# Kernel optimization log

Measured on AMD Instinct MI355X. Metric: run time of the kernel, lower is better.

## Reference

```python
import jax, jax.numpy as jnp
import numpy as np

N, E, IN_F, H, F = 4096, 131072, 512, 8, 32  # n_nodes, n_edges, in_features, n_heads, n_hidden
SLOPE = 0.2


def setup_inputs() -> dict:
    key = jax.random.key(0)
    k1, k2, k3, k4 = jax.random.split(key, 4)
    h = jax.random.normal(k1, (N, IN_F), dtype=jnp.float32)
    edge_index = jax.random.randint(k2, (2, E), 0, N)
    train_mask = jnp.ones((E + N,), dtype=jnp.float32)  # mask values written into adj (incl. self-loops appended in forward)
    W_fc = jax.random.normal(k3, (IN_F, H * F), dtype=jnp.float32) * (1.0 / np.sqrt(IN_F))
    W_attn = jax.random.normal(k4, (2 * F,), dtype=jnp.float32) * (1.0 / np.sqrt(2 * F))
    return {"h": h, "edge_index": edge_index, "train_mask": train_mask, "W_fc": W_fc, "W_attn": W_attn}


def reference(h, edge_index, train_mask, W_fc, W_attn):
    n = h.shape[0]
    g = (h @ W_fc).reshape(n, H, F)  # [n, H, F]
    # attn_fc(concat(g_i, g_j)) == g_i @ W_attn[:F] + g_j @ W_attn[F:]  (same math, no NxNx2F tensor)
    el = g @ W_attn[:F]  # [n, H], contribution of source row i
    er = g @ W_attn[F:]  # [n, H], contribution of column j
    e = jax.nn.leaky_relu(el[:, None, :] + er[None, :, :], SLOPE)  # [n, n, H]
    # adjacency: edges (+ self-loops appended in forward) get train_mask values, then diagonal forced to 1
    src = jnp.concatenate([edge_index[0], jnp.arange(n)])
    dst = jnp.concatenate([edge_index[1], jnp.arange(n)])
    adj = jnp.zeros((n, n), dtype=h.dtype).at[src, dst].set(train_mask)
    diag = jnp.arange(n)
    adj = adj.at[diag, diag].set(1.0)
    e = jnp.where(adj[:, :, None] == 0, -jnp.inf, e)
    a = jax.nn.softmax(e, axis=1)  # softmax over neighbors j (dropout p=0 -> identity)
    attn_res = jnp.einsum('ijh,jhf->ihf', a, g)  # [n, H, F]
    return attn_res.reshape(n, H * F)  # is_concat=True
```

## Files before the change

kernel.cpp:

```cpp
#include <hip/hip_runtime.h>
#include <stdint.h>

#define NN   4096
#define NE   131072
#define KIN  512
#define NH   8
#define HF   256
#define SLOPE 0.2f

typedef __attribute__((ext_vector_type(8))) short bf16x8;
typedef __attribute__((ext_vector_type(4))) float f32x4;


__device__ __forceinline__ unsigned short f2bf(float x) {
  unsigned u = __builtin_bit_cast(unsigned, x);
  u += 0x7FFFu + ((u >> 16) & 1u);
  return (unsigned short)(u >> 16);
}
__device__ __forceinline__ float bf2f(unsigned short x) {
  unsigned u = ((unsigned)x) << 16;
  return __builtin_bit_cast(float, u);
}

__global__ __launch_bounds__(256) void prep_k(const float* __restrict__ A,
                                              const float* __restrict__ B,
                                              unsigned* __restrict__ bitmap,
                                              unsigned short* __restrict__ Abf,
                                              unsigned short* __restrict__ Btbf) {
  __shared__ float tile[32][33];
  const int b = blockIdx.x, t = threadIdx.x;
  if (b < 512) {
    ((float4*)bitmap)[b * 256 + t] = make_float4(0.f, 0.f, 0.f, 0.f);
  } else if (b < 2560) {
    size_t idx = ((size_t)(b - 512) * 256 + t) * 4;
    float4 v = *(const float4*)&A[idx];
    ushort4 o;
    o.x = f2bf(v.x); o.y = f2bf(v.y); o.z = f2bf(v.z); o.w = f2bf(v.w);
    *(ushort4*)&Abf[idx] = o;
  } else {
    int bb = b - 2560;
    int k0 = (bb >> 3) * 32, n0 = (bb & 7) * 32;
    int lr = t >> 3, lc = (t & 7) * 4;
    float4 v = *(const float4*)&B[(size_t)(k0 + lr) * HF + n0 + lc];
    tile[lr][lc] = v.x; tile[lr][lc + 1] = v.y; tile[lr][lc + 2] = v.z; tile[lr][lc + 3] = v.w;
    __syncthreads();
    ushort4 o;
    o.x = f2bf(tile[lc + 0][lr]); o.y = f2bf(tile[lc + 1][lr]);
    o.z = f2bf(tile[lc + 2][lr]); o.w = f2bf(tile[lc + 3][lr]);
    *(ushort4*)&Btbf[(size_t)(n0 + lr) * KIN + k0 + lc] = o;
  }
}

__global__ __launch_bounds__(256) void gemm_adj_k(const unsigned short* __restrict__ A,
                                                  const unsigned short* __restrict__ Bt,
                                                  const float* __restrict__ Wa,
                                                  unsigned short* __restrict__ gbf,
                                                  float* __restrict__ el,
                                                  float* __restrict__ er,
                                                  const int* __restrict__ ei,
                                                  const float* __restrict__ mask,
                                                  unsigned* __restrict__ bitmap) {
  __shared__ unsigned short smem[2][8192];
  const int bx = blockIdx.x, t = threadIdx.x;
  if (bx >= 256) {
    int k = (bx - 256) * 256 + t;
    if (k < NE + NN) {
      int s, d; float m;
      if (k < NE) { s = ei[k]; d = ei[NE + k]; m = mask[k]; }
      else        { s = k - NE; d = s; m = 1.0f; }
      if (m != 0.0f) atomicOr(&bitmap[s * 128 + (d >> 5)], 1u << (d & 31));
    }
    return;
  }
  const int gx = bx & 63, gy = bx >> 6;
  const int row0 = gx * 64, col0 = gy * 64;
  const int w = t >> 6, l = t & 63;
  const int wr = w >> 1, wc = w & 1;

  const int srow = t >> 3;
  const int schunk = (t & 7) ^ (srow & 7);
  const unsigned short* gA0 = &A[(size_t)(row0 + srow) * KIN + schunk * 8];
  const unsigned short* gA1 = &A[(size_t)(row0 + 32 + srow) * KIN + schunk * 8];
  const unsigned short* gB0 = &Bt[(size_t)(col0 + srow) * KIN + schunk * 8];
  const unsigned short* gB1 = &Bt[(size_t)(col0 + 32 + srow) * KIN + schunk * 8];

#define STAGE(bf, ks)                                                                              \
  do {                                                                                             \
    __builtin_amdgcn_global_load_lds(                                                              \
        (const __attribute__((address_space(1))) unsigned int*)(gA0 + (size_t)(ks) * 64),          \
        (__attribute__((address_space(3))) unsigned int*)(&smem[bf][w * 512]), 16, 0, 0);          \
    __builtin_amdgcn_global_load_lds(                                                              \
        (const __attribute__((address_space(1))) unsigned int*)(gA1 + (size_t)(ks) * 64),          \
        (__attribute__((address_space(3))) unsigned int*)(&smem[bf][2048 + w * 512]), 16, 0, 0);   \
    __builtin_amdgcn_global_load_lds(                                                              \
        (const __attribute__((address_space(1))) unsigned int*)(gB0 + (size_t)(ks) * 64),          \
        (__attribute__((address_space(3))) unsigned int*)(&smem[bf][4096 + w * 512]), 16, 0, 0);   \
    __builtin_amdgcn_global_load_lds(                                                              \
        (const __attribute__((address_space(1))) unsigned int*)(gB1 + (size_t)(ks) * 64),          \
        (__attribute__((address_space(3))) unsigned int*)(&smem[bf][6144 + w * 512]), 16, 0, 0);   \
  } while (0)

  f32x4 acc[2][2] = {};
  STAGE(0, 0);
  __syncthreads();

  const int lrow = l & 15, kg = l >> 4;
  for (int ks = 0; ks < 8; ++ks) {
    const int bf = ks & 1;
    if (ks < 7) STAGE(bf ^ 1, ks + 1);
    bf16x8 af[2][2], bg[2][2];
#pragma unroll
    for (int r = 0; r < 2; ++r) {
      int ar = wr * 32 + r * 16 + lrow;
#pragma unroll
      for (int s = 0; s < 2; ++s)
        af[r][s] = *(const bf16x8*)&smem[bf][ar * 64 + (((s * 4 + kg) ^ (ar & 7)) << 3)];
    }
#pragma unroll
    for (int c = 0; c < 2; ++c) {
      int br = wc * 32 + c * 16 + lrow;
#pragma unroll
      for (int s = 0; s < 2; ++s)
        bg[c][s] = *(const bf16x8*)&smem[bf][4096 + br * 64 + (((s * 4 + kg) ^ (br & 7)) << 3)];
    }
#pragma unroll
    for (int s = 0; s < 2; ++s) {
      acc[0][0] = __builtin_amdgcn_mfma_f32_16x16x32_bf16(af[0][s], bg[0][s], acc[0][0], 0, 0, 0);
      acc[0][1] = __builtin_amdgcn_mfma_f32_16x16x32_bf16(af[0][s], bg[1][s], acc[0][1], 0, 0, 0);
      acc[1][0] = __builtin_amdgcn_mfma_f32_16x16x32_bf16(af[1][s], bg[0][s], acc[1][0], 0, 0, 0);
      acc[1][1] = __builtin_amdgcn_mfma_f32_16x16x32_bf16(af[1][s], bg[1][s], acc[1][1], 0, 0, 0);
    }
    __syncthreads();
  }
#undef STAGE

  const int crow = (l >> 4) * 4, ccol = l & 15;
#pragma unroll
  for (int r = 0; r < 2; ++r)
#pragma unroll
    for (int c = 0; c < 2; ++c) {
      int gc = col0 + wc * 32 + c * 16 + ccol;
#pragma unroll
      for (int q = 0; q < 4; ++q) {
        int gr = row0 + wr * 32 + r * 16 + crow + q;
        gbf[(size_t)gr * HF + gc] = f2bf(acc[r][c][q]);
      }
    }

  const int head = (gy << 1) + wc;
  const float wal0 = Wa[ccol], wal1 = Wa[ccol + 16];
  const float war0 = Wa[32 + ccol], war1 = Wa[48 + ccol];
#pragma unroll
  for (int r = 0; r < 2; ++r)
#pragma unroll
    for (int q = 0; q < 4; ++q) {
      float pel = acc[r][0][q] * wal0 + acc[r][1][q] * wal1;
      float per = acc[r][0][q] * war0 + acc[r][1][q] * war1;
#pragma unroll
      for (int m = 8; m >= 1; m >>= 1) {
        pel += __shfl_xor(pel, m);
        per += __shfl_xor(per, m);
      }
      if (ccol == 0) {
        int row = row0 + wr * 32 + r * 16 + crow + q;
        el[row * NH + head] = pel;
        er[row * NH + head] = per;
      }
    }
}

__global__ __launch_bounds__(256) void attn_k(const unsigned* __restrict__ bitmap,
                                              const unsigned short* __restrict__ gbf,
                                              const float* __restrict__ el_,
                                              const float* __restrict__ er_,
                                              float* __restrict__ out) {
  __shared__ unsigned short jl[NN];
  __shared__ int wtot[4];
  __shared__ int totalS;

  const int i = blockIdx.x;
  const int t = threadIdx.x;
  const int lane = t & 63;

  unsigned w = 0; int cnt = 0;
  if (t < 128) { w = bitmap[i * 128 + t]; cnt = __popc(w); }
  int incl = cnt;
#pragma unroll
  for (int d = 1; d < 64; d <<= 1) {
    int u = __shfl_up(incl, d);
    if (lane >= d) incl += u;
  }
  if (lane == 63) wtot[t >> 6] = incl;
  __syncthreads();
  int base = (t >= 64 && t < 128) ? wtot[0] : 0;
  if (t == 127) totalS = base + incl;
  if (t < 128) {
    int off = base + incl - cnt;
    unsigned ww = w;
    while (ww) {
      int b = __ffs(ww) - 1;
      jl[off++] = (unsigned short)(t * 32 + b);
      ww &= ww - 1;
    }
  }
  __syncthreads();
  const int total = totalS;

  const int h = t >> 5;
  const float elh = el_[i * NH + h];
  float acc0 = 0.f, den0 = 0.f, acc1 = 0.f, den1 = 0.f;
  int k = 0;
  for (; k + 2 <= total; k += 2) {
    int j0 = jl[k], j1 = jl[k + 1];
    float e0 = elh + er_[(size_t)j0 * NH + h];
    float e1 = elh + er_[(size_t)j1 * NH + h];
    float g0 = bf2f(gbf[(size_t)j0 * HF + t]);
    float g1 = bf2f(gbf[(size_t)j1 * HF + t]);
    float l0 = e0 > 0.f ? e0 : SLOPE * e0;
    float l1 = e1 > 0.f ? e1 : SLOPE * e1;
    float w0 = __expf(l0), w1 = __expf(l1);
    den0 += w0; den1 += w1;
    acc0 += w0 * g0; acc1 += w1 * g1;
  }
  if (k < total) {
    int j0 = jl[k];
    float e0 = elh + er_[(size_t)j0 * NH + h];
    float g0 = bf2f(gbf[(size_t)j0 * HF + t]);
    float l0 = e0 > 0.f ? e0 : SLOPE * e0;
    float w0 = __expf(l0);
    den0 += w0; acc0 += w0 * g0;
  }
  out[(size_t)i * HF + t] = (acc0 + acc1) / (den0 + den1);
}

extern "C" void kernel_launch(void* const* d_in, const int* in_sizes, int n_in,
                              void* d_out, int out_size, void* d_ws, size_t ws_size,
                              hipStream_t stream) {
  const float* h      = (const float*)d_in[0];
  const int*   ei     = (const int*)d_in[1];
  const float* mask   = (const float*)d_in[2];
  const float* W_fc   = (const float*)d_in[3];
  const float* W_attn = (const float*)d_in[4];
  float* out = (float*)d_out;

  char* ws = (char*)d_ws;
  unsigned* bitmap      = (unsigned*)ws;
  unsigned short* gbf   = (unsigned short*)(ws + (size_t)2 * 1024 * 1024);
  float* el             = (float*)(ws + (size_t)4 * 1024 * 1024);
  float* er             = (float*)(ws + (size_t)4 * 1024 * 1024 + 128 * 1024);
  unsigned short* Abf   = (unsigned short*)(ws + (size_t)4 * 1024 * 1024 + 256 * 1024);
  unsigned short* Btbf  = (unsigned short*)(ws + (size_t)8 * 1024 * 1024 + 256 * 1024);

  prep_k<<<2688, 256, 0, stream>>>(h, W_fc, bitmap, Abf, Btbf);
  gemm_adj_k<<<256 + 528, 256, 0, stream>>>(Abf, Btbf, W_attn, gbf, el, er, ei, mask, bitmap);
  attn_k<<<NN, 256, 0, stream>>>(bitmap, gbf, el, er, out);
}
```

Measured before the change: 39.26 us.

## Shrink GEMM tiles to 32x32 and precompute attention weights per chunk in LDS

The GEMM moves from 64x64 to 32x32 tiles, giving 1024 blocks instead of 256 so more of the GPU is busy. Each wave now holds one 16x16 accumulator, and the el/er per-head reduction is finished through shared memory. In the attention kernel, the leaky-relu and exp weights for each chunk of 256 neighbours across all 8 heads are computed cooperatively into LDS, so each exp is evaluated once instead of 32 times per head. The gather loop is unrolled by four. The cost is that smaller tiles load A and B from memory more often, and the attention chunks need extra barriers.

```diff
diff --git a/kernel.cpp b/kernel.cpp
--- a/kernel.cpp
+++ b/kernel.cpp
@@ -60,113 +60,78 @@
                                                   const int* __restrict__ ei,
                                                   const float* __restrict__ mask,
                                                   unsigned* __restrict__ bitmap) {
-  __shared__ unsigned short smem[2][8192];
+  __shared__ unsigned short smem[2][4096];
   const int bx = blockIdx.x, t = threadIdx.x;
-  if (bx >= 256) {
-    int k = (bx - 256) * 256 + t;
-    if (k < NE + NN) {
-      int s, d; float m;
-      if (k < NE) { s = ei[k]; d = ei[NE + k]; m = mask[k]; }
-      else        { s = k - NE; d = s; m = 1.0f; }
-      if (m != 0.0f) atomicOr(&bitmap[s * 128 + (d >> 5)], 1u << (d & 31));
-    }
+  if (bx >= 1024) {
+    int k = (bx - 1024) * 256 + t;
+    int s, d; float m;
+    if (k < NE) { s = ei[k]; d = ei[NE + k]; m = mask[k]; }
+    else        { s = k - NE; d = s; m = 1.0f; }
+    if (m != 0.0f) atomicOr(&bitmap[s * 128 + (d >> 5)], 1u << (d & 31));
     return;
   }
-  const int gx = bx & 63, gy = bx >> 6;
-  const int row0 = gx * 64, col0 = gy * 64;
+  const int gx = bx & 127, gy = bx >> 7;
+  const int row0 = gx * 32, col0 = gy * 32;
   const int w = t >> 6, l = t & 63;
   const int wr = w >> 1, wc = w & 1;
 
-  const int srow = t >> 3;
-  const int schunk = (t & 7) ^ (srow & 7);
-  const unsigned short* gA0 = &A[(size_t)(row0 + srow) * KIN + schunk * 8];
-  const unsigned short* gA1 = &A[(size_t)(row0 + 32 + srow) * KIN + schunk * 8];
-  const unsigned short* gB0 = &Bt[(size_t)(col0 + srow) * KIN + schunk * 8];
-  const unsigned short* gB1 = &Bt[(size_t)(col0 + 32 + srow) * KIN + schunk * 8];
-
-#define STAGE(bf, ks)                                                                              \
-  do {                                                                                             \
-    __builtin_amdgcn_global_load_lds(                                                              \
-        (const __attribute__((address_space(1))) unsigned int*)(gA0 + (size_t)(ks) * 64),          \
-        (__attribute__((address_space(3))) unsigned int*)(&smem[bf][w * 512]), 16, 0, 0);          \
-    __builtin_amdgcn_global_load_lds(                                                              \
-        (const __attribute__((address_space(1))) unsigned int*)(gA1 + (size_t)(ks) * 64),          \
-        (__attribute__((address_space(3))) unsigned int*)(&smem[bf][2048 + w * 512]), 16, 0, 0);   \
-    __builtin_amdgcn_global_load_lds(                                                              \
-        (const __attribute__((address_space(1))) unsigned int*)(gB0 + (size_t)(ks) * 64),          \
-        (__attribute__((address_space(3))) unsigned int*)(&smem[bf][4096 + w * 512]), 16, 0, 0);   \
-    __builtin_amdgcn_global_load_lds(                                                              \
-        (const __attribute__((address_space(1))) unsigned int*)(gB1 + (size_t)(ks) * 64),          \
-        (__attribute__((address_space(3))) unsigned int*)(&smem[bf][6144 + w * 512]), 16, 0, 0);   \
+  const int srow = (w << 3) + (l >> 3);
+  const int sch  = (l & 7) ^ (srow & 7);
+  const unsigned short* gA = &A[(size_t)(row0 + srow) * KIN + sch * 8];
+  const unsigned short* gB = &Bt[(size_t)(col0 + srow) * KIN + sch * 8];
+
+#define STAGE(bf, ks)                                                                             \
+  do {                                                                                            \
+    __builtin_amdgcn_global_load_lds(                                                             \
+        (const __attribute__((address_space(1))) unsigned int*)(gA + (size_t)(ks) * 64),          \
+        (__attribute__((address_space(3))) unsigned int*)(&smem[bf][w * 512]), 16, 0, 0);         \
+    __builtin_amdgcn_global_load_lds(                                                             \
+        (const __attribute__((address_space(1))) unsigned int*)(gB + (size_t)(ks) * 64),          \
+        (__attribute__((address_space(3))) unsigned int*)(&smem[bf][2048 + w * 512]), 16, 0, 0);  \
   } while (0)
 
-  f32x4 acc[2][2] = {};
+  f32x4 acc = {};
   STAGE(0, 0);
   __syncthreads();
-
   const int lrow = l & 15, kg = l >> 4;
+  const int ar = wr * 16 + lrow, br = wc * 16 + lrow;
   for (int ks = 0; ks < 8; ++ks) {
     const int bf = ks & 1;
     if (ks < 7) STAGE(bf ^ 1, ks + 1);
-    bf16x8 af[2][2], bg[2][2];
-#pragma unroll
-    for (int r = 0; r < 2; ++r) {
-      int ar = wr * 32 + r * 16 + lrow;
-#pragma unroll
-      for (int s = 0; s < 2; ++s)
-        af[r][s] = *(const bf16x8*)&smem[bf][ar * 64 + (((s * 4 + kg) ^ (ar & 7)) << 3)];
-    }
-#pragma unroll
-    for (int c = 0; c < 2; ++c) {
-      int br = wc * 32 + c * 16 + lrow;
-#pragma unroll
-      for (int s = 0; s < 2; ++s)
-        bg[c][s] = *(const bf16x8*)&smem[bf][4096 + br * 64 + (((s * 4 + kg) ^ (br & 7)) << 3)];
-    }
-#pragma unroll
-    for (int s = 0; s < 2; ++s) {
-      acc[0][0] = __builtin_amdgcn_mfma_f32_16x16x32_bf16(af[0][s], bg[0][s], acc[0][0], 0, 0, 0);
-      acc[0][1] = __builtin_amdgcn_mfma_f32_16x16x32_bf16(af[0][s], bg[1][s], acc[0][1], 0, 0, 0);
-      acc[1][0] = __builtin_amdgcn_mfma_f32_16x16x32_bf16(af[1][s], bg[0][s], acc[1][0], 0, 0, 0);
-      acc[1][1] = __builtin_amdgcn_mfma_f32_16x16x32_bf16(af[1][s], bg[1][s], acc[1][1], 0, 0, 0);
-    }
+    bf16x8 a0 = *(const bf16x8*)&smem[bf][ar * 64 + ((kg ^ (ar & 7)) << 3)];
+    bf16x8 a1 = *(const bf16x8*)&smem[bf][ar * 64 + (((4 + kg) ^ (ar & 7)) << 3)];
+    bf16x8 b0 = *(const bf16x8*)&smem[bf][2048 + br * 64 + ((kg ^ (br & 7)) << 3)];
+    bf16x8 b1 = *(const bf16x8*)&smem[bf][2048 + br * 64 + (((4 + kg) ^ (br & 7)) << 3)];
+    acc = __builtin_amdgcn_mfma_f32_16x16x32_bf16(a0, b0, acc, 0, 0, 0);
+    acc = __builtin_amdgcn_mfma_f32_16x16x32_bf16(a1, b1, acc, 0, 0, 0);
     __syncthreads();
   }
 #undef STAGE
 
   const int crow = (l >> 4) * 4, ccol = l & 15;
-#pragma unroll
-  for (int r = 0; r < 2; ++r)
-#pragma unroll
-    for (int c = 0; c < 2; ++c) {
-      int gc = col0 + wc * 32 + c * 16 + ccol;
-#pragma unroll
-      for (int q = 0; q < 4; ++q) {
-        int gr = row0 + wr * 32 + r * 16 + crow + q;
-        gbf[(size_t)gr * HF + gc] = f2bf(acc[r][c][q]);
-      }
-    }
-
-  const int head = (gy << 1) + wc;
-  const float wal0 = Wa[ccol], wal1 = Wa[ccol + 16];
-  const float war0 = Wa[32 + ccol], war1 = Wa[48 + ccol];
-#pragma unroll
-  for (int r = 0; r < 2; ++r)
-#pragma unroll
-    for (int q = 0; q < 4; ++q) {
-      float pel = acc[r][0][q] * wal0 + acc[r][1][q] * wal1;
-      float per = acc[r][0][q] * war0 + acc[r][1][q] * war1;
-#pragma unroll
-      for (int m = 8; m >= 1; m >>= 1) {
-        pel += __shfl_xor(pel, m);
-        per += __shfl_xor(per, m);
-      }
-      if (ccol == 0) {
-        int row = row0 + wr * 32 + r * 16 + crow + q;
-        el[row * NH + head] = pel;
-        er[row * NH + head] = per;
-      }
-    }
+  const int gr0 = row0 + wr * 16 + crow, gc = col0 + wc * 16 + ccol;
+#pragma unroll
+  for (int q = 0; q < 4; ++q) gbf[(size_t)(gr0 + q) * HF + gc] = f2bf(acc[q]);
+
+  float* red = (float*)smem;
+  const int f = wc * 16 + ccol;
+  const float wal = Wa[f], war = Wa[32 + f];
+#pragma unroll
+  for (int q = 0; q < 4; ++q) {
+    float pel = acc[q] * wal, per = acc[q] * war;
+#pragma unroll
+    for (int m = 8; m >= 1; m >>= 1) { pel += __shfl_xor(pel, m); per += __shfl_xor(per, m); }
+    if (ccol == 0) {
+      int rl = wr * 16 + crow + q;
+      red[wc * 32 + rl] = pel;
+      red[64 + wc * 32 + rl] = per;
+    }
+  }
+  __syncthreads();
+  if (t < 32) {
+    el[(row0 + t) * NH + gy] = red[t] + red[32 + t];
+    er[(row0 + t) * NH + gy] = red[64 + t] + red[96 + t];
+  }
 }
 
 __global__ __launch_bounds__(256) void attn_k(const unsigned* __restrict__ bitmap,
@@ -175,6 +140,7 @@
                                               const float* __restrict__ er_,
                                               float* __restrict__ out) {
   __shared__ unsigned short jl[NN];
+  __shared__ float wlds[256 * NH];
   __shared__ int wtot[4];
   __shared__ int totalS;
 
@@ -182,8 +148,8 @@
   const int t = threadIdx.x;
   const int lane = t & 63;
 
-  unsigned w = 0; int cnt = 0;
-  if (t < 128) { w = bitmap[i * 128 + t]; cnt = __popc(w); }
+  unsigned wbits = 0; int cnt = 0;
+  if (t < 128) { wbits = bitmap[i * 128 + t]; cnt = __popc(wbits); }
   int incl = cnt;
 #pragma unroll
   for (int d = 1; d < 64; d <<= 1) {
@@ -196,7 +162,7 @@
   if (t == 127) totalS = base + incl;
   if (t < 128) {
     int off = base + incl - cnt;
-    unsigned ww = w;
+    unsigned ww = wbits;
     while (ww) {
       int b = __ffs(ww) - 1;
       jl[off++] = (unsigned short)(t * 32 + b);
@@ -206,31 +172,39 @@
   __syncthreads();
   const int total = totalS;
 
-  const int h = t >> 5;
-  const float elh = el_[i * NH + h];
-  float acc0 = 0.f, den0 = 0.f, acc1 = 0.f, den1 = 0.f;
-  int k = 0;
-  for (; k + 2 <= total; k += 2) {
-    int j0 = jl[k], j1 = jl[k + 1];
-    float e0 = elh + er_[(size_t)j0 * NH + h];
-    float e1 = elh + er_[(size_t)j1 * NH + h];
-    float g0 = bf2f(gbf[(size_t)j0 * HF + t]);
-    float g1 = bf2f(gbf[(size_t)j1 * HF + t]);
-    float l0 = e0 > 0.f ? e0 : SLOPE * e0;
-    float l1 = e1 > 0.f ? e1 : SLOPE * e1;
-    float w0 = __expf(l0), w1 = __expf(l1);
-    den0 += w0; den1 += w1;
-    acc0 += w0 * g0; acc1 += w1 * g1;
-  }
-  if (k < total) {
-    int j0 = jl[k];
-    float e0 = elh + er_[(size_t)j0 * NH + h];
-    float g0 = bf2f(gbf[(size_t)j0 * HF + t]);
-    float l0 = e0 > 0.f ? e0 : SLOPE * e0;
-    float w0 = __expf(l0);
-    den0 += w0; acc0 += w0 * g0;
-  }
-  out[(size_t)i * HF + t] = (acc0 + acc1) / (den0 + den1);
+  const int hh = t >> 5;
+  float acc = 0.f, den = 0.f;
+  for (int c0 = 0; c0 < total; c0 += 256) {
+    const int CL = min(256, total - c0);
+    for (int p = t; p < CL * NH; p += 256) {
+      int k = p >> 3, h2 = p & 7;
+      int j = jl[c0 + k];
+      float e  = el_[i * NH + h2] + er_[(size_t)j * NH + h2];
+      float lr = e > 0.f ? e : SLOPE * e;
+      wlds[p] = __expf(lr);
+    }
+    __syncthreads();
+    int k = 0;
+    for (; k + 4 <= CL; k += 4) {
+      int j0 = jl[c0 + k], j1 = jl[c0 + k + 1], j2 = jl[c0 + k + 2], j3 = jl[c0 + k + 3];
+      float g0 = bf2f(gbf[(size_t)j0 * HF + t]);
+      float g1 = bf2f(gbf[(size_t)j1 * HF + t]);
+      float g2 = bf2f(gbf[(size_t)j2 * HF + t]);
+      float g3 = bf2f(gbf[(size_t)j3 * HF + t]);
+      float w0 = wlds[(k + 0) * NH + hh], w1 = wlds[(k + 1) * NH + hh];
+      float w2 = wlds[(k + 2) * NH + hh], w3 = wlds[(k + 3) * NH + hh];
+      den += (w0 + w1) + (w2 + w3);
+      acc += w0 * g0; acc += w1 * g1; acc += w2 * g2; acc += w3 * g3;
+    }
+    for (; k < CL; ++k) {
+      int j0 = jl[c0 + k];
+      float w0 = wlds[k * NH + hh];
+      den += w0;
+      acc += w0 * bf2f(gbf[(size_t)j0 * HF + t]);
+    }
+    __syncthreads();
+  }
+  out[(size_t)i * HF + t] = acc / den;
 }
 
 extern "C" void kernel_launch(void* const* d_in, const int* in_sizes, int n_in,
@@ -252,6 +226,6 @@
   unsigned short* Btbf  = (unsigned short*)(ws + (size_t)8 * 1024 * 1024 + 256 * 1024);
 
   prep_k<<<2688, 256, 0, stream>>>(h, W_fc, bitmap, Abf, Btbf);
-  gemm_adj_k<<<256 + 528, 256, 0, stream>>>(Abf, Btbf, W_attn, gbf, el, er, ei, mask, bitmap);
+  gemm_adj_k<<<1024 + 528, 256, 0, stream>>>(Abf, Btbf, W_attn, gbf, el, er, ei, mask, bitmap);
   attn_k<<<NN, 256, 0, stream>>>(bitmap, gbf, el, er, out);
 }
```

Measured after the change: 37.03 us. -5.7%, faster.
